# Kernel optimization log

Hardware: AMD Instinct MI355X
Metric: run time of the kernel (lower is better)

## Reference

```python
import jax, jax.numpy as jnp
import numpy as np

ALPHA, BETA, GAMMA = 1.0, 1.0, 0.7
WIN = 11
C1 = 0.01 ** 2
C2 = 0.03 ** 2


def get_sobel_kernels(n1=1, n2=2, n3=2):
    a = np.asarray
    Sx = a([[[-n1, 0, n1], [-n2, 0, n2], [-n1, 0, n1]],
            [[-n2, 0, n2], [-n3 * n2, 0, n3 * n2], [-n2, 0, n2]],
            [[-n1, 0, n1], [-n2, 0, n2], [-n1, 0, n1]]])
    Sy = a([[[-n1, -n2, -n1], [0, 0, 0], [n1, n2, n1]],
            [[-n2, -n3 * n2, -n2], [0, 0, 0], [n2, n3 * n2, n2]],
            [[-n1, -n2, -n1], [0, 0, 0], [n1, n2, n1]]])
    Sz = a([[[-n1, -n2, -n1], [-n2, -n3 * n2, -n2], [-n1, -n2, -n1]],
            [[0, 0, 0], [0, 0, 0], [0, 0, 0]],
            [[n1, n2, n1], [n2, n3 * n2, n2], [n1, n2, n1]]])
    Sd11 = a([[[0, n1, n2], [-n1, 0, n1], [-n2, -n1, 0]],
              [[0, n2, n2 * n3], [-n2, 0, n2], [-n2 * n3, -n2, 0]],
              [[0, n1, n2], [-n1, 0, n1], [-n2, -n1, 0]]])
    Sd12 = a([[[-n2, -n1, 0], [-n1, 0, n1], [0, n1, n2]],
              [[-n2 * n3, -n2, 0], [-n2, 0, n2], [0, n2, n2 * n3]],
              [[-n2, -n1, 0], [-n1, 0, n1], [0, n1, n2]]])
    Sd21 = Sd11.T
    Sd22 = Sd12.T
    Sd31 = a([-S.T for S in Sd11.T])
    Sd32 = a([S.T for S in Sd12.T])
    return np.stack([Sx, Sy, Sz, Sd11, Sd12, Sd21, Sd22, Sd31, Sd32]).astype(np.float32)

# (9,1,3,3,3) fused sobel bank -- single grouped conv instead of 9 launches
SOBEL_W = jnp.asarray(get_sobel_kernels()[:, None])


def _gauss1d():
    g = jnp.exp(-(jnp.arange(WIN, dtype=jnp.float32) - WIN // 2) ** 2 / (2 * 1.5 ** 2))
    return g / g.sum()

G1D = _gauss1d()


def conv3d(x, w):
    return jax.lax.conv_general_dilated(
        x, w, window_strides=(1, 1, 1), padding='SAME',
        dimension_numbers=('NCDHW', 'OIDHW', 'NCDHW'))


def gauss_filter(x):
    # separable 11-tap gaussian along D, H, W (== full 11^3 window, zero-padded SAME)
    x = conv3d(x, G1D.reshape(1, 1, WIN, 1, 1))
    x = conv3d(x, G1D.reshape(1, 1, 1, WIN, 1))
    x = conv3d(x, G1D.reshape(1, 1, 1, 1, WIN))
    return x


def edge_map(img):
    # GradEdge3D.__call__ with a=1, C=1
    B, C, D, H, W = img.shape
    xp = jnp.pad(img, ((0, 0), (0, 0), (1, 1), (1, 1), (1, 1)), mode='reflect')
    g = conv3d(xp, SOBEL_W)                       # (B, 9, D+2, H+2, W+2)
    gm = jnp.sqrt(jnp.sum((g + 1e-6) ** 2 + 1e-6, axis=1))  # (B, D+2, H+2, W+2)
    gm = gm[:, 1:-1, 1:-1, 1:-1]
    norm = (gm - gm.min()) / (gm.max() - gm.min() + 1e-6)
    return norm.reshape(B, 1, D, H, W)


def ssim_value(pred, target):
    mu_p = gauss_filter(pred)
    mu_t = gauss_filter(target)
    mu_p2, mu_t2, mu_pt = mu_p ** 2, mu_t ** 2, mu_p * mu_t
    sig_p = gauss_filter(pred * pred) - mu_p2
    sig_t = gauss_filter(target * target) - mu_t2
    sig_pt = gauss_filter(pred * target) - mu_pt
    ssim_map = ((2 * mu_pt + C1) * (2 * sig_pt + C2)) / ((mu_p2 + mu_t2 + C1) * (sig_p + sig_t + C2))
    return 1.0 - ssim_map.mean()


def setup_inputs() -> dict:
    key = jax.random.key(0)
    k1, k2 = jax.random.split(key)
    shape = (2, 1, 128, 128, 128)
    return {
        'pred': jax.random.uniform(k1, shape, dtype=jnp.float32),
        'target': jax.random.uniform(k2, shape, dtype=jnp.float32),
    }


def reference(pred, target):
    loss_mse = jnp.mean((pred - target) ** 2)
    loss_ssim = ssim_value(pred, target)
    # GMELoss3D: lam_errors=[(1.0, L1Loss())], reduction='sum'
    loss_gme = 1e-6 + jnp.mean(jnp.abs(edge_map(pred) - edge_map(target)))
    total = ALPHA * loss_mse + BETA * loss_ssim + GAMMA * loss_gme
    return (total, loss_mse, loss_ssim, loss_gme)
```

## Files before the change

### kernel.cpp

```cpp
#include <hip/hip_runtime.h>


#define VOL 4194304
#define HV  2097152

typedef _Float16 h2 __attribute__((ext_vector_type(2)));
typedef _Float16 h8 __attribute__((ext_vector_type(8)));

constexpr float GW[11] = {
    0.00102838f, 0.00759876f, 0.03600077f, 0.10936070f, 0.21300554f,
    0.26601173f,
    0.21300554f, 0.10936070f, 0.03600077f, 0.00759876f, 0.00102838f};


__global__ __launch_bounds__(256) void k_init(double* dbl, unsigned int* ui) {
  const int tid = threadIdx.x + (blockIdx.x << 8);
  if (tid < 1536) dbl[tid] = 0.0;
  if (tid < 4096) ui[tid] = (tid < 2048) ? 0x7F800000u : 0u;
}

__device__ __forceinline__ void wblur_body(
    const float* __restrict__ p, const float* __restrict__ t,
    _Float16* __restrict__ A, double* __restrict__ mseB, const int bidx) {
  __shared__ float sr[2][138];
  __shared__ float dr[2][138];
  __shared__ float redw[256];
  const int tid = threadIdx.x;
  const int rl = tid >> 7;
  const int x  = tid & 127;
  const int rowBase = bidx << 4;
  if (x < 5)    { sr[rl][x] = 0.f;      dr[rl][x] = 0.f; }
  if (x >= 123) { sr[rl][10 + x] = 0.f; dr[rl][10 + x] = 0.f; }
  float pv = p[((rowBase + rl) << 7) + x];
  float tv = t[((rowBase + rl) << 7) + x];
  float msel = 0.f;
  for (int it = 0; it < 8; ++it) {
    const int row  = rowBase + (it << 1) + rl;
    const int base = row << 7;
    const float sv = pv + tv;
    const float dv = pv - tv;
    sr[rl][5 + x] = sv; dr[rl][5 + x] = dv;
    msel += dv * dv;
    __syncthreads();
    float pvN = 0.f, tvN = 0.f;
    if (it < 7) {
      const int baseN = (row + 2) << 7;
      pvN = p[baseN + x]; tvN = t[baseN + x];
    }
    float as = 0.f, ad = 0.f, ass = 0.f, add_ = 0.f;
#pragma unroll
    for (int k = 0; k < 11; ++k) {
      const float w = GW[k];
      const float a = sr[rl][x + k];
      const float b = dr[rl][x + k];
      const float wa = w * a;
      const float wb = w * b;
      as += wa; ad += wb;
      ass += wa * a; add_ += wb * b;
    }
    const int idx = base + x;
    A[idx]           = (_Float16)as;
    A[VOL + idx]     = (_Float16)ad;
    A[2 * VOL + idx] = (_Float16)ass;
    A[3 * VOL + idx] = (_Float16)add_;
    __syncthreads();
    pv = pvN; tv = tvN;
  }
  redw[tid] = msel;
  __syncthreads();
  for (int s = 128; s > 0; s >>= 1) {
    if (tid < s) redw[tid] += redw[tid + s];
    __syncthreads();
  }
  if (tid == 0) atomicAdd(&mseB[(bidx & 63) << 3], (double)redw[0]);
}

__device__ __forceinline__ void sobel_body(
    const float* __restrict__ p, const float* __restrict__ t,
    _Float16* __restrict__ gmP, _Float16* __restrict__ gmT,
    unsigned int* __restrict__ ui, const int bx, const int by, const int bz) {
  __shared__ float sb[1296];
  __shared__ float rmin[256];
  __shared__ float rmax[256];
  const int tid = threadIdx.x;
  const int tx = tid & 15;
  const int ty = tid >> 4;
  const int x0 = bx << 4;
  const int y0 = by << 4;
  const int vol = bz >> 3;
  const int b   = (bz >> 2) & 1;
  const int z0  = (bz & 3) << 5;
  const float* __restrict__ img = vol ? t : p;
  _Float16* __restrict__ gm = vol ? gmT : gmP;
  const int vb = b << 21;

  const int l1 = tid;
  const int ly1 = l1 / 18, lx1 = l1 % 18;
  const int la1 = ly1 * 24 + lx1;
  int gy1 = y0 - 1 + ly1; gy1 = gy1 < 0 ? 1 : (gy1 > 127 ? 126 : gy1);
  int gx1 = x0 - 1 + lx1; gx1 = gx1 < 0 ? 1 : (gx1 > 127 ? 126 : gx1);
  const int off1 = (gy1 << 7) + gx1;
  const int l2 = tid + 256;
  const int ly2 = l2 / 18, lx2 = l2 % 18;
  const int la2 = ly2 * 24 + lx2;
  int gy2 = y0 - 1 + ly2; gy2 = gy2 < 0 ? 1 : (gy2 > 127 ? 126 : gy2);
  int gx2 = x0 - 1 + lx2; gx2 = gx2 < 0 ? 1 : (gx2 > 127 ? 126 : gx2);
  const int off2 = (gy2 << 7) + gx2;
  const bool has2 = (tid < 68);
  const int rb = ty * 24 + tx;
  const int gbase = vb + (z0 << 14) + ((y0 + ty) << 7) + (x0 + tx);

  float Y0[7], Y1[7], Y2[7];
  float rv1 = 0.f, rv2 = 0.f;
  float lmin = 3.4e38f, lmax = 0.f;

#define LOADR(ZS) {                                                         \
    const int zc_ = (ZS) > 127 ? 126 : (ZS);                                \
    const int za_ = vb + (zc_ << 14);                                       \
    rv1 = img[za_ + off1];                                                  \
    if (has2) rv2 = img[za_ + off2]; }

#define WRITELDS(BOFF) {                                                    \
    sb[(BOFF) + la1] = rv1;                                                 \
    if (has2) sb[(BOFF) + la2] = rv2; }

#define COMPY(P) {                                                          \
    const int o_ = (P) * 432 + rb;                                          \
    const float r00 = sb[o_],      r01 = sb[o_ + 1],  r02 = sb[o_ + 2];     \
    const float r10 = sb[o_ + 24], r11 = sb[o_ + 25], r12 = sb[o_ + 26];    \
    const float r20 = sb[o_ + 48], r21 = sb[o_ + 49], r22 = sb[o_ + 50];    \
    const float dx0 = r02 - r00, dx1 = r12 - r10, dx2 = r22 - r20;          \
    const float ux0 = r00 + r01 + r02, ux1 = r10 + r11 + r12,               \
                ux2 = r20 + r21 + r22;                                      \
    const float sx0 = ux0 + r01, sx1 = ux1 + r11, sx2 = ux2 + r21;          \
    Y##P[1] = dx0 + dx1 + dx2;                                    \
    Y##P[0] = Y##P[1] + dx1;                                      \
    Y##P[2] = sx2 - sx0;                                          \
    Y##P[4] = sx0 + sx1 + sx2;                                    \
    Y##P[3] = Y##P[4] + sx1;                                      \
    Y##P[5] = ux2 - ux0;                                          \
    Y##P[6] = (ux0 + ux2) + 2.f * ux1; }

#define EMIT(I, P0, P1, P2) {                                               \
    const float E_ = Y##P0[0] + Y##P1[0] + Y##P2[0];                        \
    const float g1 = E_ + Y##P1[0];                                         \
    const float tA = Y##P0[1] + Y##P1[1] + Y##P2[1];                        \
    const float A_ = tA + Y##P1[1];                                         \
    const float D_ = Y##P0[2] + Y##P1[2] + Y##P2[2];                        \
    const float g2 = D_ + Y##P1[2];                                         \
    const float g3 = Y##P2[3] - Y##P0[3];                                   \
    const float C_ = Y##P2[4] - Y##P0[4];                                   \
    const float B_ = (Y##P0[5] + Y##P2[5]) + 2.f * Y##P1[5];                \
    const float F_ = Y##P2[6] - Y##P0[6];                                   \
    const float g4 = A_ - B_, g5 = A_ + B_;                                 \
    const float g6 = C_ - D_, g7 = C_ + D_;                                 \
    const float g8 = E_ - F_, g9 = E_ + F_;                                 \
    float ss_ = 9e-6f, t_;                                                  \
    t_ = g1 + 1e-6f; ss_ = fmaf(t_, t_, ss_);                               \
    t_ = g2 + 1e-6f; ss_ = fmaf(t_, t_, ss_);                               \
    t_ = g3 + 1e-6f; ss_ = fmaf(t_, t_, ss_);                               \
    t_ = g4 + 1e-6f; ss_ = fmaf(t_, t_, ss_);                               \
    t_ = g5 + 1e-6f; ss_ = fmaf(t_, t_, ss_);                               \
    t_ = g6 + 1e-6f; ss_ = fmaf(t_, t_, ss_);                               \
    t_ = g7 + 1e-6f; ss_ = fmaf(t_, t_, ss_);                               \
    t_ = g8 + 1e-6f; ss_ = fmaf(t_, t_, ss_);                               \
    t_ = g9 + 1e-6f; ss_ = fmaf(t_, t_, ss_);                               \
    const _Float16 gh = (_Float16)sqrtf(ss_);                               \
    gm[gbase + ((I) << 14)] = gh;                                           \
    const float gq = (float)gh;                                             \
    lmin = fminf(lmin, gq); lmax = fmaxf(lmax, gq); }

#define BODY(I, P0, P1, P2) {                                               \
    WRITELDS((P2) * 432);                                                   \
    LOADR(z0 + (I) + 2);                                                    \
    __syncthreads();                                                        \
    COMPY(P2);                                                              \
    EMIT(I, P0, P1, P2); }

  {
    const int zp = (z0 == 0) ? 1 : (z0 - 1);
    LOADR(zp);  WRITELDS(0);
    LOADR(z0);  WRITELDS(432);
    __syncthreads();
    COMPY(0);
    COMPY(1);
    LOADR(z0 + 1);
  }
  for (int ii = 0; ii < 30; ii += 3) {
    BODY(ii,     0, 1, 2);
    BODY(ii + 1, 1, 2, 0);
    BODY(ii + 2, 2, 0, 1);
  }
  BODY(30, 0, 1, 2);
  BODY(31, 1, 2, 0);

#undef BODY
#undef EMIT
#undef COMPY
#undef WRITELDS
#undef LOADR

  rmin[tid] = lmin; rmax[tid] = lmax;
  __syncthreads();
  for (int st = 128; st > 0; st >>= 1) {
    if (tid < st) {
      rmin[tid] = fminf(rmin[tid], rmin[tid + st]);
      rmax[tid] = fmaxf(rmax[tid], rmax[tid + st]);
    }
    __syncthreads();
  }
  if (tid == 0) {
    const int bin = (bx + (by << 3) + (bz << 6)) & 63;
    atomicMin(&ui[vol * 1024 + (bin << 4)], __float_as_uint(rmin[0]));
    atomicMax(&ui[2048 + vol * 1024 + (bin << 4)], __float_as_uint(rmax[0]));
  }
}

__device__ __forceinline__ void blury_body(
    const _Float16* __restrict__ A, _Float16* __restrict__ B,
    const int z, const int yseg, const int batch) {
  __shared__ h8 s[4][26][16];
  const int tid = threadIdx.x;
  const int y0 = yseg << 4;
  const int b8 = batch << 18;
  const h8* __restrict__ Ah = (const h8*)A;
  h8* __restrict__ Bh = (h8*)B;
  const int slice8 = b8 + (z << 11);
  for (int q = 0; q < 4; ++q) {
    const h8* __restrict__ Aq = Ah + (q << 19) + slice8;
    for (int l = tid; l < 416; l += 256) {
      const int row = l >> 4, xc = l & 15;
      const int y = y0 - 5 + row;
      h8 v{};
      if ((unsigned)y < 128u) v = Aq[(y << 4) + xc];
      s[q][row][xc] = v;
    }
  }
  __syncthreads();
  const int xc = tid & 15;
  const int yo = tid >> 4;
  const int wbase = slice8 + ((y0 + yo) << 4) + xc;
#pragma unroll
  for (int q = 0; q < 4; ++q) {
    h8 acc{};
#pragma unroll
    for (int k = 0; k < 11; ++k) {
      const _Float16 w = (_Float16)GW[k];
      acc += w * s[q][yo + k][xc];
    }
    Bh[(q << 19) + wbase] = acc;
  }
}

__device__ __forceinline__ void edge_body(
    const _Float16* __restrict__ gmP, const _Float16* __restrict__ gmT,
    const unsigned int* __restrict__ ui, double* __restrict__ absB,
    const int bidx) {
  __shared__ float rede[256];
  float mnp = 3.4e38f, mnt = 3.4e38f, mxp = 0.f, mxt = 0.f;
  for (int j = 0; j < 64; ++j) {
    mnp = fminf(mnp, __uint_as_float(ui[j << 4]));
    mnt = fminf(mnt, __uint_as_float(ui[1024 + (j << 4)]));
    mxp = fmaxf(mxp, __uint_as_float(ui[2048 + (j << 4)]));
    mxt = fmaxf(mxt, __uint_as_float(ui[3072 + (j << 4)]));
  }
  const float scp = 1.f / (mxp - mnp + 1e-6f);
  const float sct = 1.f / (mxt - mnt + 1e-6f);
  const h8* __restrict__ gp = (const h8*)gmP;
  const h8* __restrict__ gt = (const h8*)gmT;
  float lsum = 0.f;
  const int base = bidx << 9;
#pragma unroll
  for (int i = 0; i < 2; ++i) {
    const int idx = base + (i << 8) + threadIdx.x;
    const h8 a = gp[idx];
    const h8 b = gt[idx];
#pragma unroll
    for (int j = 0; j < 8; ++j)
      lsum += fabsf(((float)a[j] - mnp) * scp - ((float)b[j] - mnt) * sct);
  }
  rede[threadIdx.x] = lsum;
  __syncthreads();
  for (int s = 128; s > 0; s >>= 1) {
    if (threadIdx.x < s) rede[threadIdx.x] += rede[threadIdx.x + s];
    __syncthreads();
  }
  if (threadIdx.x == 0)
    atomicAdd(&absB[(bidx & 63) << 3], (double)rede[0]);
}

__global__ __launch_bounds__(256) void k_fused_a(
    const float* __restrict__ p, const float* __restrict__ t,
    _Float16* __restrict__ A, double* __restrict__ mseB,
    _Float16* __restrict__ gmP, _Float16* __restrict__ gmT,
    unsigned int* __restrict__ ui) {
  const int bid = blockIdx.x;
  const int r3 = bid % 3;
  if (r3 < 2) {
    wblur_body(p, t, A, mseB, (bid / 3) * 2 + r3);
  } else {
    const int s = bid / 3;
    sobel_body(p, t, gmP, gmT, ui, s & 7, (s >> 3) & 7, s >> 6);
  }
}

__global__ __launch_bounds__(256) void k_fused_b(
    const _Float16* __restrict__ A, _Float16* __restrict__ B,
    const _Float16* __restrict__ gmP, const _Float16* __restrict__ gmT,
    const unsigned int* __restrict__ ui, double* __restrict__ absB) {
  const int bid = blockIdx.x;
  const int r3 = bid % 3;
  if (r3 < 2) {
    const int idx = (bid / 3) * 2 + r3;
    blury_body(A, B, idx & 127, (idx >> 7) & 7, idx >> 10);
  } else {
    edge_body(gmP, gmT, ui, absB, bid / 3);
  }
}

__global__ __launch_bounds__(256) void k_zblur_ssim(
    const _Float16* __restrict__ B, double* __restrict__ ssimB) {
  __shared__ h8 s[4][26][16];
  __shared__ float red[256];
  const int tid = threadIdx.x;
  const int y  = blockIdx.x;
  const int z0 = blockIdx.y << 4;
  const int b8 = blockIdx.z << 18;
  const h8* __restrict__ Bh = (const h8*)B;
  const int col8 = b8 + (y << 4);
  for (int q = 0; q < 4; ++q) {
    const h8* __restrict__ Bq = Bh + (q << 19) + col8;
    for (int l = tid; l < 416; l += 256) {
      const int row = l >> 4, xc = l & 15;
      const int zz = z0 - 5 + row;
      h8 v{};
      if ((unsigned)zz < 128u) v = Bq[(zz << 11) + xc];
      s[q][row][xc] = v;
    }
  }
  __syncthreads();
  const int xc = tid & 15;
  const int zo = tid >> 4;
  h8 m[4];
#pragma unroll
  for (int q = 0; q < 4; ++q) {
    h8 acc{};
#pragma unroll
    for (int k = 0; k < 11; ++k) {
      const _Float16 w = (_Float16)GW[k];
      acc += w * s[q][zo + k][xc];
    }
    m[q] = acc;
  }
  float lsum = 0.f;
#pragma unroll
  for (int j = 0; j < 8; ++j) {
    const float mus = (float)m[0][j];
    const float mud = (float)m[1][j];
    const float ess = (float)m[2][j];
    const float edd = (float)m[3][j];
    const float S2 = mus * mus, D2 = mud * mud;
    const float num = ((S2 - D2) * 0.5f + 1e-4f) *
                      ((ess - edd - S2 + D2) * 0.5f + 9e-4f);
    const float den = ((S2 + D2) * 0.5f + 1e-4f) *
                      ((ess + edd - S2 - D2) * 0.5f + 9e-4f);
    lsum += num / den;
  }
  red[tid] = lsum;
  __syncthreads();
  for (int st = 128; st > 0; st >>= 1) {
    if (tid < st) red[tid] += red[tid + st];
    __syncthreads();
  }
  if (tid == 0) {
    const int bin = (blockIdx.x + (blockIdx.y << 3) + blockIdx.z) & 63;
    atomicAdd(&ssimB[bin << 3], (double)red[0]);
  }
}

__global__ void k_final(const double* __restrict__ dbl, float* __restrict__ out) {
  if (threadIdx.x == 0 && blockIdx.x == 0) {
    double ms = 0.0, ss = 0.0, ab = 0.0;
    for (int j = 0; j < 64; ++j) {
      ms += dbl[j << 3];
      ss += dbl[512 + (j << 3)];
      ab += dbl[1024 + (j << 3)];
    }
    const double N = 4194304.0;
    const double mse   = ms / N;
    const double ssiml = 1.0 - ss / N;
    const double gme   = 1e-6 + ab / N;
    const double total = mse + ssiml + 0.7 * gme;
    out[0] = (float)total;
    out[1] = (float)mse;
    out[2] = (float)ssiml;
    out[3] = (float)gme;
  }
}

extern "C" void kernel_launch(void* const* d_in, const int* in_sizes, int n_in,
                              void* d_out, int out_size, void* d_ws, size_t ws_size,
                              hipStream_t stream) {
  const float* p = (const float*)d_in[0];
  const float* t = (const float*)d_in[1];
  _Float16* A = (_Float16*)d_ws;
  _Float16* B = A + (size_t)4 * VOL;
  char* accb = (char*)d_ws + (size_t)20 * VOL;
  double* dbl = (double*)accb;
  unsigned int* ui = (unsigned int*)(accb + 12288);
  _Float16* gmP = (_Float16*)((char*)d_ws + 88080384);
  _Float16* gmT = gmP + VOL;
  float* out = (float*)d_out;

  k_init<<<16, 256, 0, stream>>>(dbl, ui);
  k_fused_a<<<3072, 256, 0, stream>>>(p, t, A, dbl, gmP, gmT, ui);
  k_fused_b<<<3072, 256, 0, stream>>>(A, B, gmP, gmT, ui, dbl + 1024);
  k_zblur_ssim<<<dim3(128, 8, 2), 256, 0, stream>>>(B, dbl + 512);
  k_final<<<1, 64, 0, stream>>>(dbl, out);
}
```

Before: 150.8 us.

## Halve sobel z-chunk, interleave 1:1 with blur, fold init and final into memset/last-block

The sobel blocks now each cover 16 z-slices instead of 32, doubling their count, and are interleaved 1:1 with the W-blur blocks in a 4096-block grid for better load balance. The halo loads switch to a direct 24-stride mapping with validity masks. The min reduction is encoded as atomicMax on the bit-inverted value, so the accumulators can be zeroed by a single hipMemsetAsync instead of an init kernel. The final-reduction kernel is removed and its work is done by the last block of the SSIM kernel, found through an atomic counter. This removes two launches at the cost of more halo reloads and a threadfence/counter pattern.

After: 238.0 us. +57.9%, slower.

```diff
diff --git a/kernel.cpp b/kernel.cpp
--- a/kernel.cpp
+++ b/kernel.cpp
@@ -12,12 +12,6 @@
     0.26601173f,
     0.21300554f, 0.10936070f, 0.03600077f, 0.00759876f, 0.00102838f};
 
-
-__global__ __launch_bounds__(256) void k_init(double* dbl, unsigned int* ui) {
-  const int tid = threadIdx.x + (blockIdx.x << 8);
-  if (tid < 1536) dbl[tid] = 0.0;
-  if (tid < 4096) ui[tid] = (tid < 2048) ? 0x7F800000u : 0u;
-}
 
 __device__ __forceinline__ void wblur_body(
     const float* __restrict__ p, const float* __restrict__ t,
@@ -87,26 +81,24 @@
   const int ty = tid >> 4;
   const int x0 = bx << 4;
   const int y0 = by << 4;
-  const int vol = bz >> 3;
-  const int b   = (bz >> 2) & 1;
-  const int z0  = (bz & 3) << 5;
+  const int vol = bz >> 4;
+  const int b   = (bz >> 3) & 1;
+  const int z0  = (bz & 7) << 4;
   const float* __restrict__ img = vol ? t : p;
   _Float16* __restrict__ gm = vol ? gmT : gmP;
   const int vb = b << 21;
 
-  const int l1 = tid;
-  const int ly1 = l1 / 18, lx1 = l1 % 18;
-  const int la1 = ly1 * 24 + lx1;
+  const int ly1 = tid / 24, lx1 = tid % 24;
+  const bool v1 = (lx1 < 18);
   int gy1 = y0 - 1 + ly1; gy1 = gy1 < 0 ? 1 : (gy1 > 127 ? 126 : gy1);
   int gx1 = x0 - 1 + lx1; gx1 = gx1 < 0 ? 1 : (gx1 > 127 ? 126 : gx1);
   const int off1 = (gy1 << 7) + gx1;
-  const int l2 = tid + 256;
-  const int ly2 = l2 / 18, lx2 = l2 % 18;
-  const int la2 = ly2 * 24 + lx2;
+  const int s2i = tid + 256;
+  const int ly2 = s2i / 24, lx2 = s2i % 24;
+  const bool v2 = (s2i < 432) && (lx2 < 18);
   int gy2 = y0 - 1 + ly2; gy2 = gy2 < 0 ? 1 : (gy2 > 127 ? 126 : gy2);
   int gx2 = x0 - 1 + lx2; gx2 = gx2 < 0 ? 1 : (gx2 > 127 ? 126 : gx2);
   const int off2 = (gy2 << 7) + gx2;
-  const bool has2 = (tid < 68);
   const int rb = ty * 24 + tx;
   const int gbase = vb + (z0 << 14) + ((y0 + ty) << 7) + (x0 + tx);
 
@@ -117,12 +109,12 @@
 #define LOADR(ZS) {                                                         \
     const int zc_ = (ZS) > 127 ? 126 : (ZS);                                \
     const int za_ = vb + (zc_ << 14);                                       \
-    rv1 = img[za_ + off1];                                                  \
-    if (has2) rv2 = img[za_ + off2]; }
+    if (v1) rv1 = img[za_ + off1];                                          \
+    if (v2) rv2 = img[za_ + off2]; }
 
 #define WRITELDS(BOFF) {                                                    \
-    sb[(BOFF) + la1] = rv1;                                                 \
-    if (has2) sb[(BOFF) + la2] = rv2; }
+    if (v1) sb[(BOFF) + tid] = rv1;                                         \
+    if (v2) sb[(BOFF) + s2i] = rv2; }
 
 #define COMPY(P) {                                                          \
     const int o_ = (P) * 432 + rb;                                          \
@@ -186,13 +178,12 @@
     COMPY(1);
     LOADR(z0 + 1);
   }
-  for (int ii = 0; ii < 30; ii += 3) {
+  for (int ii = 0; ii < 15; ii += 3) {
     BODY(ii,     0, 1, 2);
     BODY(ii + 1, 1, 2, 0);
     BODY(ii + 2, 2, 0, 1);
   }
-  BODY(30, 0, 1, 2);
-  BODY(31, 1, 2, 0);
+  BODY(15, 0, 1, 2);
 
 #undef BODY
 #undef EMIT
@@ -211,7 +202,7 @@
   }
   if (tid == 0) {
     const int bin = (bx + (by << 3) + (bz << 6)) & 63;
-    atomicMin(&ui[vol * 1024 + (bin << 4)], __float_as_uint(rmin[0]));
+    atomicMax(&ui[vol * 1024 + (bin << 4)], ~__float_as_uint(rmin[0]));
     atomicMax(&ui[2048 + vol * 1024 + (bin << 4)], __float_as_uint(rmax[0]));
   }
 }
@@ -257,13 +248,21 @@
     const unsigned int* __restrict__ ui, double* __restrict__ absB,
     const int bidx) {
   __shared__ float rede[256];
-  float mnp = 3.4e38f, mnt = 3.4e38f, mxp = 0.f, mxt = 0.f;
+  unsigned umnp = 0u, umnt = 0u, umxp = 0u, umxt = 0u;
   for (int j = 0; j < 64; ++j) {
-    mnp = fminf(mnp, __uint_as_float(ui[j << 4]));
-    mnt = fminf(mnt, __uint_as_float(ui[1024 + (j << 4)]));
-    mxp = fmaxf(mxp, __uint_as_float(ui[2048 + (j << 4)]));
-    mxt = fmaxf(mxt, __uint_as_float(ui[3072 + (j << 4)]));
-  }
+    const unsigned a0 = ui[j << 4];
+    const unsigned a1 = ui[1024 + (j << 4)];
+    const unsigned a2 = ui[2048 + (j << 4)];
+    const unsigned a3 = ui[3072 + (j << 4)];
+    umnp = umnp > a0 ? umnp : a0;
+    umnt = umnt > a1 ? umnt : a1;
+    umxp = umxp > a2 ? umxp : a2;
+    umxt = umxt > a3 ? umxt : a3;
+  }
+  const float mnp = __uint_as_float(~umnp);
+  const float mnt = __uint_as_float(~umnt);
+  const float mxp = __uint_as_float(umxp);
+  const float mxt = __uint_as_float(umxt);
   const float scp = 1.f / (mxp - mnp + 1e-6f);
   const float sct = 1.f / (mxt - mnt + 1e-6f);
   const h8* __restrict__ gp = (const h8*)gmP;
@@ -295,11 +294,10 @@
     _Float16* __restrict__ gmP, _Float16* __restrict__ gmT,
     unsigned int* __restrict__ ui) {
   const int bid = blockIdx.x;
-  const int r3 = bid % 3;
-  if (r3 < 2) {
-    wblur_body(p, t, A, mseB, (bid / 3) * 2 + r3);
+  if ((bid & 1) == 0) {
+    wblur_body(p, t, A, mseB, bid >> 1);
   } else {
-    const int s = bid / 3;
+    const int s = bid >> 1;
     sobel_body(p, t, gmP, gmT, ui, s & 7, (s >> 3) & 7, s >> 6);
   }
 }
@@ -319,7 +317,8 @@
 }
 
 __global__ __launch_bounds__(256) void k_zblur_ssim(
-    const _Float16* __restrict__ B, double* __restrict__ ssimB) {
+    const _Float16* __restrict__ B, double* __restrict__ dbl,
+    unsigned int* __restrict__ cnt, float* __restrict__ out) {
   __shared__ h8 s[4][26][16];
   __shared__ float red[256];
   const int tid = threadIdx.x;
@@ -374,27 +373,27 @@
   }
   if (tid == 0) {
     const int bin = (blockIdx.x + (blockIdx.y << 3) + blockIdx.z) & 63;
-    atomicAdd(&ssimB[bin << 3], (double)red[0]);
-  }
-}
-
-__global__ void k_final(const double* __restrict__ dbl, float* __restrict__ out) {
-  if (threadIdx.x == 0 && blockIdx.x == 0) {
-    double ms = 0.0, ss = 0.0, ab = 0.0;
-    for (int j = 0; j < 64; ++j) {
-      ms += dbl[j << 3];
-      ss += dbl[512 + (j << 3)];
-      ab += dbl[1024 + (j << 3)];
-    }
-    const double N = 4194304.0;
-    const double mse   = ms / N;
-    const double ssiml = 1.0 - ss / N;
-    const double gme   = 1e-6 + ab / N;
-    const double total = mse + ssiml + 0.7 * gme;
-    out[0] = (float)total;
-    out[1] = (float)mse;
-    out[2] = (float)ssiml;
-    out[3] = (float)gme;
+    atomicAdd(&dbl[512 + (bin << 3)], (double)red[0]);
+    __threadfence();
+    const unsigned prev = atomicAdd(cnt, 1u);
+    if (prev == 2047u) {
+      double ms = 0.0, ss = 0.0, ab = 0.0;
+#pragma unroll
+      for (int j = 0; j < 64; ++j) {
+        ms += atomicAdd(&dbl[j << 3], 0.0);
+        ss += atomicAdd(&dbl[512 + (j << 3)], 0.0);
+        ab += atomicAdd(&dbl[1024 + (j << 3)], 0.0);
+      }
+      const double N = 4194304.0;
+      const double mse   = ms / N;
+      const double ssiml = 1.0 - ss / N;
+      const double gme   = 1e-6 + ab / N;
+      const double total = mse + ssiml + 0.7 * gme;
+      out[0] = (float)total;
+      out[1] = (float)mse;
+      out[2] = (float)ssiml;
+      out[3] = (float)gme;
+    }
   }
 }
 
@@ -408,13 +407,13 @@
   char* accb = (char*)d_ws + (size_t)20 * VOL;
   double* dbl = (double*)accb;
   unsigned int* ui = (unsigned int*)(accb + 12288);
+  unsigned int* cnt = (unsigned int*)(accb + 28672);
   _Float16* gmP = (_Float16*)((char*)d_ws + 88080384);
   _Float16* gmT = gmP + VOL;
   float* out = (float*)d_out;
 
-  k_init<<<16, 256, 0, stream>>>(dbl, ui);
-  k_fused_a<<<3072, 256, 0, stream>>>(p, t, A, dbl, gmP, gmT, ui);
+  hipMemsetAsync(accb, 0, 28676, stream);
+  k_fused_a<<<4096, 256, 0, stream>>>(p, t, A, dbl, gmP, gmT, ui);
   k_fused_b<<<3072, 256, 0, stream>>>(A, B, gmP, gmT, ui, dbl + 1024);
-  k_zblur_ssim<<<dim3(128, 8, 2), 256, 0, stream>>>(B, dbl + 512);
-  k_final<<<1, 64, 0, stream>>>(dbl, out);
-}
+  k_zblur_ssim<<<dim3(128, 8, 2), 256, 0, stream>>>(B, dbl, cnt, out);
+}
```
